# Kernel optimization log

Hardware: AMD Instinct MI355X
Metric: run time of the kernel (lower is better)

Reference implementation:

```python
import jax, jax.numpy as jnp
import numpy as np
from jax import lax

B, T_CAP, V, WD, H, L, IC = 256, 51, 10000, 512, 512, 2, 2048


def setup_inputs() -> dict:
    key = jax.random.key(0)
    ks = jax.random.split(key, 16)
    u01 = lambda k, s: jax.random.uniform(k, s, jnp.float32, -0.1, 0.1)
    sc = 1.0 / np.sqrt(H)
    uh = lambda k, s: jax.random.uniform(k, s, jnp.float32, -sc, sc)
    image_code = jax.random.normal(ks[0], (B, IC), jnp.float32)
    captions = jax.random.randint(ks[1], (B, T_CAP), 0, V)
    cap_lens = jax.random.randint(ks[2], (B,), 2, T_CAP + 1)
    cap_lens = cap_lens.at[0].set(T_CAP)  # guarantees max len == T_CAP (static scan length)
    return {
        "image_code": image_code,
        "captions": captions,
        "cap_lens": cap_lens,
        "embed_w": u01(ks[3], (V, WD)),
        "init_w": uh(ks[4], (L * H, IC)),
        "init_b": uh(ks[5], (L * H,)),
        "w_ih0": uh(ks[6], (3 * H, WD + IC)),
        "w_hh0": uh(ks[7], (3 * H, H)),
        "b_ih0": uh(ks[8], (3 * H,)),
        "b_hh0": uh(ks[9], (3 * H,)),
        "w_ih1": uh(ks[10], (3 * H, H)),
        "w_hh1": uh(ks[11], (3 * H, H)),
        "b_ih1": uh(ks[12], (3 * H,)),
        "b_hh1": uh(ks[13], (3 * H,)),
        "fc_w": u01(ks[14], (V, H)),
        "fc_b": jnp.zeros((V,), jnp.float32),
    }


def _gru_cell(x, h, w_ih, w_hh, b_ih, b_hh):
    # torch nn.GRU cell: gates ordered (r, z, n)
    gi = x @ w_ih.T + b_ih
    gh = h @ w_hh.T + b_hh
    i_r, i_z, i_n = jnp.split(gi, 3, axis=-1)
    h_r, h_z, h_n = jnp.split(gh, 3, axis=-1)
    r = jax.nn.sigmoid(i_r + h_r)
    z = jax.nn.sigmoid(i_z + h_z)
    n = jnp.tanh(i_n + r * h_n)
    return (1.0 - z) * n + z * h


def reference(image_code, captions, cap_lens, embed_w, init_w, init_b,
              w_ih0, w_hh0, b_ih0, b_hh0, w_ih1, w_hh1, b_ih1, b_hh1,
              fc_w, fc_b):
    b = image_code.shape[0]
    # sort by caption length, descending (ragged batch shrink in original)
    order = jnp.argsort(-cap_lens)
    sorted_lens = cap_lens[order]
    caps = captions[order]
    img = image_code[order]
    # init hidden: (L, B, H)
    h0 = (img @ init_w.T + init_b).reshape(b, L, H).transpose(1, 0, 2)
    lengths = sorted_lens - 1                      # decode steps per example
    T = captions.shape[1] - 1                      # static; equals lengths[0] by construction
    emb = embed_w[caps]                            # (B, T+1, WD)
    xs = jnp.swapaxes(emb[:, :T, :], 0, 1)         # (T, B, WD)
    mask_ts = jnp.arange(T)[:, None] < lengths[None, :]  # (T, B)
    params = [(w_ih0, w_hh0, b_ih0, b_hh0), (w_ih1, w_hh1, b_ih1, b_hh1)]

    def step(h, inp):
        x_emb, m = inp
        layer_in = jnp.concatenate([img, x_emb], axis=-1)  # (B, IC+WD)
        new_h = []
        for l, (wi, wh, bi, bh) in enumerate(params):
            hl = _gru_cell(layer_in, h[l], wi, wh, bi, bh)
            new_h.append(hl)
            layer_in = hl
        h_new = jnp.stack(new_h)
        # rows past their length keep their old hidden (equivalent to the
        # torch loop never touching rows beyond real_batch_size)
        h_new = jnp.where(m[None, :, None], h_new, h)
        preds = layer_in @ fc_w.T + fc_b           # dropout is identity in eval
        preds = jnp.where(m[:, None], preds, 0.0)  # predictions stay zero past length
        return h_new, preds

    _, preds = lax.scan(step, h0, (xs, mask_ts))   # preds: (T, B, V)
    predictions = jnp.swapaxes(preds, 0, 1)        # (B, T, V)
    return predictions, caps, lengths, order
```

## Files before the change

### kernel.cpp

```cpp
#include <hip/hip_runtime.h>
#include <hip/hip_bf16.h>

#define BB   256
#define TCAP 51
#define TT   50
#define VV   10000
#define WDIM 512
#define HH   512
#define ICC  2048
#define G3H  1536
#define FCP  8

typedef __attribute__((ext_vector_type(8))) short short8v;
typedef __attribute__((ext_vector_type(4))) float f32x4;

__device__ __forceinline__ unsigned short f2bf(float f) {
    unsigned u; __builtin_memcpy(&u, &f, 4);
    unsigned r = (u + 0x7FFFu + ((u >> 16) & 1u)) >> 16;
    return (unsigned short)r;
}
__device__ __forceinline__ float bf2f(unsigned short b) {
    unsigned u = ((unsigned)b) << 16; float f; __builtin_memcpy(&f, &u, 4); return f;
}
__device__ __forceinline__ short8v cvt8(float4 a, float4 b) {
    union { unsigned short u[8]; short8v v; } o;
    o.u[0] = f2bf(a.x); o.u[1] = f2bf(a.y); o.u[2] = f2bf(a.z); o.u[3] = f2bf(a.w);
    o.u[4] = f2bf(b.x); o.u[5] = f2bf(b.y); o.u[6] = f2bf(b.z); o.u[7] = f2bf(b.w);
    return o.v;
}
__device__ __forceinline__ float sigm(float x) { return 1.f / (1.f + expf(-x)); }

__global__ void sort_kernel(const int* __restrict__ cap_lens, const int* __restrict__ captions,
                            int* __restrict__ order_ws, int* __restrict__ len_ws,
                            int* __restrict__ caps_ws, float* __restrict__ out,
                            size_t predN) {
    __shared__ int s_order[BB];
    int i = threadIdx.x;
    int li = cap_lens[i];
    int rank = 0;
    for (int j = 0; j < BB; ++j) {
        int lj = cap_lens[j];
        rank += (lj > li) || (lj == li && j < i);
    }
    s_order[rank] = i;
    __syncthreads();
    int src = s_order[i];
    order_ws[i] = src;
    int len = cap_lens[src] - 1;
    len_ws[i] = len;
    for (int t = 0; t < TCAP; ++t) {
        int c = captions[src * TCAP + t];
        caps_ws[i * TCAP + t] = c;
        out[predN + (size_t)i * TCAP + t] = (float)c;
    }
    out[predN + (size_t)BB * TCAP + i]      = (float)len;
    out[predN + (size_t)BB * TCAP + BB + i] = (float)src;
}

__global__ void gather_imgb(const float* __restrict__ image_code, const int* __restrict__ order_ws,
                            unsigned short* __restrict__ imgb) {
    int i = blockIdx.x * 256 + threadIdx.x;
    int p = i >> 8, c8 = (i & 255) << 3;
    const float* s = image_code + (size_t)order_ws[p] * ICC + c8;
    float4 v0 = *(const float4*)s, v1 = *(const float4*)(s + 4);
    *(short8v*)&imgb[(size_t)p * ICC + c8] = cvt8(v0, v1);
}

__global__ void cvt_mat(const float* __restrict__ src, int src_ld, int src_off,
                        unsigned short* __restrict__ dst, int dst_ld, int dst_off,
                        int cols, int n8) {
    int i = blockIdx.x * 256 + threadIdx.x;
    if (i < n8) {
        int cpr = cols >> 3;
        int row = i / cpr, c8 = (i - row * cpr) << 3;
        const float* s = src + (size_t)row * src_ld + src_off + c8;
        float4 v0 = *(const float4*)s, v1 = *(const float4*)(s + 4);
        *(short8v*)&dst[(size_t)row * dst_ld + dst_off + c8] = cvt8(v0, v1);
    }
}

__global__ __launch_bounds__(256) void gemm_front(
    const unsigned short* __restrict__ imgb,
    const unsigned short* __restrict__ wcomb,
    const float* __restrict__ init_b,
    const float* __restrict__ b_ih0,
    unsigned short* __restrict__ h0s0,
    unsigned short* __restrict__ h1s0,
    float* __restrict__ gi_img) {
    const int p0 = blockIdx.y * 64;
    const int c0 = blockIdx.x * 64;
    const int tid = threadIdx.x;
    __shared__ unsigned short As[64][64 + FCP], Bs[64][64 + FCP];
    const int lane = tid & 63, w = tid >> 6;
    f32x4 acc[4] = {};
    for (int k0 = 0; k0 < ICC; k0 += 64) {
#pragma unroll
        for (int v = 0; v < 2; ++v) {
            int e = tid + v * 256;
            int rr = e >> 3, kk = (e & 7) * 8;
            *(short8v*)&As[rr][kk] = *(const short8v*)&imgb[(size_t)(p0 + rr) * ICC + k0 + kk];
            *(short8v*)&Bs[rr][kk] = *(const short8v*)&wcomb[(size_t)(c0 + rr) * ICC + k0 + kk];
        }
        __syncthreads();
#pragma unroll
        for (int ks = 0; ks < 64; ks += 32) {
            short8v a = *(const short8v*)&As[w * 16 + (lane & 15)][ks + (lane >> 4) * 8];
#pragma unroll
            for (int n = 0; n < 4; ++n) {
                short8v b = *(const short8v*)&Bs[n * 16 + (lane & 15)][ks + (lane >> 4) * 8];
                acc[n] = __builtin_amdgcn_mfma_f32_16x16x32_bf16(a, b, acc[n], 0, 0, 0);
            }
        }
        __syncthreads();
    }
#pragma unroll
    for (int n = 0; n < 4; ++n) {
        int cc = c0 + n * 16 + (lane & 15);
#pragma unroll
        for (int r = 0; r < 4; ++r) {
            int pr = p0 + w * 16 + (lane >> 4) * 4 + r;
            float v = acc[n][r];
            if (cc < 1024) {
                v += init_b[cc];
                unsigned short b = f2bf(v);
                if (cc < 512) h0s0[(size_t)pr * 512 + cc] = b;
                else          h1s0[(size_t)pr * 512 + (cc - 512)] = b;
            } else {
                gi_img[(size_t)pr * G3H + (cc - 1024)] = v + b_ih0[cc - 1024];
            }
        }
    }
}

__global__ __launch_bounds__(256) void gemm_giemb(
    const unsigned short* __restrict__ embb,
    const unsigned short* __restrict__ wihe,
    const float* __restrict__ gi_img,
    const int* __restrict__ caps_ws, const int* __restrict__ len_ws,
    float* __restrict__ gi_all) {
    const int r0 = blockIdx.y * 64;
    const int t = r0 >> 8, p0 = r0 & 255;
    if (len_ws[p0] <= t) return;
    const int c0 = blockIdx.x * 64;
    const int tid = threadIdx.x;
    __shared__ unsigned short As[64][64 + FCP], Bs[64][64 + FCP];
    __shared__ int s_arow[64];
    if (tid < 64) s_arow[tid] = caps_ws[(p0 + tid) * TCAP + t];
    __syncthreads();
    const int lane = tid & 63, w = tid >> 6;
    f32x4 acc[4] = {};
    for (int k0 = 0; k0 < WDIM; k0 += 64) {
#pragma unroll
        for (int v = 0; v < 2; ++v) {
            int e = tid + v * 256;
            int rr = e >> 3, kk = (e & 7) * 8;
            *(short8v*)&As[rr][kk] = *(const short8v*)&embb[(size_t)s_arow[rr] * WDIM + k0 + kk];
            *(short8v*)&Bs[rr][kk] = *(const short8v*)&wihe[(size_t)(c0 + rr) * WDIM + k0 + kk];
        }
        __syncthreads();
#pragma unroll
        for (int ks = 0; ks < 64; ks += 32) {
            short8v a = *(const short8v*)&As[w * 16 + (lane & 15)][ks + (lane >> 4) * 8];
#pragma unroll
            for (int n = 0; n < 4; ++n) {
                short8v b = *(const short8v*)&Bs[n * 16 + (lane & 15)][ks + (lane >> 4) * 8];
                acc[n] = __builtin_amdgcn_mfma_f32_16x16x32_bf16(a, b, acc[n], 0, 0, 0);
            }
        }
        __syncthreads();
    }
#pragma unroll
    for (int n = 0; n < 4; ++n) {
        int cc = c0 + n * 16 + (lane & 15);
#pragma unroll
        for (int r = 0; r < 4; ++r) {
            int pr = p0 + w * 16 + (lane >> 4) * 4 + r;
            if (t < len_ws[pr])
                gi_all[((size_t)t * BB + pr) * G3H + cc] = acc[n][r] + gi_img[(size_t)pr * G3H + cc];
        }
    }
}

__global__ __launch_bounds__(256) void gru_stage(int s,
    const unsigned short* __restrict__ h0_rd, unsigned short* __restrict__ h0_wr,
    float* __restrict__ gx_wr, const float* __restrict__ gx_rd,
    const unsigned short* __restrict__ h1_rd, unsigned short* __restrict__ h1_wr,
    unsigned short* __restrict__ h1x,
    const unsigned short* __restrict__ whh0b,
    const unsigned short* __restrict__ wih1b,
    const unsigned short* __restrict__ whh1b,
    const float* __restrict__ b_hh0, const float* __restrict__ gi_all,
    const float* __restrict__ b_ih1, const float* __restrict__ b_hh1,
    const int* __restrict__ len_ws) {
    const int role = blockIdx.x >> 5;
    const int sub = blockIdx.x & 31;
    const int cc0 = (sub & 7) * 64;
    const int p0 = (sub >> 3) * 64;
    const int t = s - role;
    if (t < 0 || t >= TT) return;
    if (len_ws[p0] <= t) return;
    const int tid = threadIdx.x, lane = tid & 63, w = tid >> 6;
    __shared__ unsigned short As[64][72];
    __shared__ unsigned short Bs[3][64][72];
    const unsigned short* Arows = (role == 2) ? h1_rd : h0_rd;
    const unsigned short* Bw = (role == 0) ? whh0b : (role == 1) ? wih1b : whh1b;
    const int rr0 = tid >> 3, kk0 = (tid & 7) * 8;
    f32x4 aG0[4] = {}, aG1[4] = {}, aG2[4] = {};
    short8v pa0, pa1, pb00, pb01, pb02, pb10, pb11, pb12;

#define LOADK(KC) {                                                                  \
    size_t ko = (size_t)(KC) * 64 + kk0;                                             \
    pa0  = *(const short8v*)&Arows[(size_t)(p0 + rr0) * 512 + ko];                   \
    pa1  = *(const short8v*)&Arows[(size_t)(p0 + rr0 + 32) * 512 + ko];              \
    pb00 = *(const short8v*)&Bw[(size_t)(cc0 + rr0) * 512 + ko];                     \
    pb01 = *(const short8v*)&Bw[(size_t)(512 + cc0 + rr0) * 512 + ko];               \
    pb02 = *(const short8v*)&Bw[(size_t)(1024 + cc0 + rr0) * 512 + ko];              \
    pb10 = *(const short8v*)&Bw[(size_t)(cc0 + rr0 + 32) * 512 + ko];                \
    pb11 = *(const short8v*)&Bw[(size_t)(512 + cc0 + rr0 + 32) * 512 + ko];          \
    pb12 = *(const short8v*)&Bw[(size_t)(1024 + cc0 + rr0 + 32) * 512 + ko]; }

    LOADK(0);
    for (int kc = 0; kc < 8; ++kc) {
        if (kc) __syncthreads();
        *(short8v*)&As[rr0][kk0] = pa0;
        *(short8v*)&As[rr0 + 32][kk0] = pa1;
        *(short8v*)&Bs[0][rr0][kk0] = pb00;
        *(short8v*)&Bs[1][rr0][kk0] = pb01;
        *(short8v*)&Bs[2][rr0][kk0] = pb02;
        *(short8v*)&Bs[0][rr0 + 32][kk0] = pb10;
        *(short8v*)&Bs[1][rr0 + 32][kk0] = pb11;
        *(short8v*)&Bs[2][rr0 + 32][kk0] = pb12;
        __syncthreads();
        if (kc < 7) LOADK(kc + 1);
#pragma unroll
        for (int ks = 0; ks < 64; ks += 32) {
            short8v a = *(const short8v*)&As[w * 16 + (lane & 15)][ks + (lane >> 4) * 8];
#pragma unroll
            for (int n = 0; n < 4; ++n) {
                int br = n * 16 + (lane & 15), bk = ks + (lane >> 4) * 8;
                short8v b0 = *(const short8v*)&Bs[0][br][bk];
                aG0[n] = __builtin_amdgcn_mfma_f32_16x16x32_bf16(a, b0, aG0[n], 0, 0, 0);
                short8v b1 = *(const short8v*)&Bs[1][br][bk];
                aG1[n] = __builtin_amdgcn_mfma_f32_16x16x32_bf16(a, b1, aG1[n], 0, 0, 0);
                short8v b2 = *(const short8v*)&Bs[2][br][bk];
                aG2[n] = __builtin_amdgcn_mfma_f32_16x16x32_bf16(a, b2, aG2[n], 0, 0, 0);
            }
        }
    }
#undef LOADK

    if (role == 0) {
#pragma unroll
        for (int n = 0; n < 4; ++n) {
            int cc = cc0 + n * 16 + (lane & 15);
            float bR = b_hh0[cc], bZ = b_hh0[512 + cc], bN = b_hh0[1024 + cc];
#pragma unroll
            for (int r = 0; r < 4; ++r) {
                int p = p0 + w * 16 + (lane >> 4) * 4 + r;
                const float* gi = gi_all + ((size_t)t * BB + p) * G3H;
                float rr_ = sigm(gi[cc] + aG0[n][r] + bR);
                float zz  = sigm(gi[512 + cc] + aG1[n][r] + bZ);
                float nn  = tanhf(gi[1024 + cc] + rr_ * (aG2[n][r] + bN));
                float hold = bf2f(h0_rd[(size_t)p * 512 + cc]);
                float hnew = (t < len_ws[p]) ? (1.f - zz) * nn + zz * hold : hold;
                h0_wr[(size_t)p * 512 + cc] = f2bf(hnew);
            }
        }
    } else if (role == 1) {
#pragma unroll
        for (int n = 0; n < 4; ++n) {
            int cc = cc0 + n * 16 + (lane & 15);
            float bR = b_ih1[cc], bZ = b_ih1[512 + cc], bN = b_ih1[1024 + cc];
#pragma unroll
            for (int r = 0; r < 4; ++r) {
                int p = p0 + w * 16 + (lane >> 4) * 4 + r;
                float* gx = gx_wr + (size_t)p * G3H;
                gx[cc]        = aG0[n][r] + bR;
                gx[512 + cc]  = aG1[n][r] + bZ;
                gx[1024 + cc] = aG2[n][r] + bN;
            }
        }
    } else {
#pragma unroll
        for (int n = 0; n < 4; ++n) {
            int cc = cc0 + n * 16 + (lane & 15);
            float bR = b_hh1[cc], bZ = b_hh1[512 + cc], bN = b_hh1[1024 + cc];
#pragma unroll
            for (int r = 0; r < 4; ++r) {
                int p = p0 + w * 16 + (lane >> 4) * 4 + r;
                const float* gx = gx_rd + (size_t)p * G3H;
                float rr_ = sigm(gx[cc] + aG0[n][r] + bR);
                float zz  = sigm(gx[512 + cc] + aG1[n][r] + bZ);
                float nn  = tanhf(gx[1024 + cc] + rr_ * (aG2[n][r] + bN));
                float hold = bf2f(h1_rd[(size_t)p * 512 + cc]);
                float hnew = (t < len_ws[p]) ? (1.f - zz) * nn + zz * hold : hold;
                unsigned short hb = f2bf(hnew);
                h1_wr[(size_t)p * 512 + cc] = hb;
                h1x[((size_t)t * BB + p) * 512 + cc] = hb;
            }
        }
    }
}

__global__ __launch_bounds__(256) void gemm_fc_mfma(
    const unsigned short* __restrict__ h1x,
    const unsigned short* __restrict__ fcwb,
    const float* __restrict__ fc_b,
    const int* __restrict__ len_ws,
    float* __restrict__ out) {
    const int r0 = blockIdx.y * 64;
    const int t = r0 >> 8, p0 = r0 & 255;
    const int c0 = blockIdx.x * 64;
    const int tid = threadIdx.x;
    if (len_ws[p0] <= t) {
        for (int e = tid; e < 64 * 16; e += 256) {
            int rl = e >> 4, c = c0 + (e & 15) * 4;
            if (c < VV) {
                float4 z = {0.f, 0.f, 0.f, 0.f};
                *(float4*)&out[((size_t)(p0 + rl) * TT + t) * VV + c] = z;
            }
        }
        return;
    }
    __shared__ unsigned short As[64][64 + FCP];
    __shared__ unsigned short Bs[64][64 + FCP];
    const int lane = tid & 63, w = tid >> 6;
    f32x4 acc[4] = {};
    for (int k0 = 0; k0 < HH; k0 += 64) {
#pragma unroll
        for (int v = 0; v < 2; ++v) {
            int e = tid + v * 256;
            int rr = e >> 3, kk = (e & 7) * 8;
            *(short8v*)&As[rr][kk] =
                *(const short8v*)&h1x[((size_t)(t * BB + p0 + rr)) * HH + k0 + kk];
            int bc = c0 + rr;
            short8v bv = {};
            if (bc < VV) bv = *(const short8v*)&fcwb[(size_t)bc * HH + k0 + kk];
            *(short8v*)&Bs[rr][kk] = bv;
        }
        __syncthreads();
#pragma unroll
        for (int ks = 0; ks < 64; ks += 32) {
            short8v a = *(const short8v*)&As[w * 16 + (lane & 15)][ks + (lane >> 4) * 8];
#pragma unroll
            for (int n = 0; n < 4; ++n) {
                short8v b = *(const short8v*)&Bs[n * 16 + (lane & 15)][ks + (lane >> 4) * 8];
                acc[n] = __builtin_amdgcn_mfma_f32_16x16x32_bf16(a, b, acc[n], 0, 0, 0);
            }
        }
        __syncthreads();
    }
#pragma unroll
    for (int n = 0; n < 4; ++n) {
        int c = c0 + n * 16 + (lane & 15);
        if (c < VV) {
            float bias = fc_b[c];
#pragma unroll
            for (int r = 0; r < 4; ++r) {
                int pr = p0 + w * 16 + (lane >> 4) * 4 + r;
                bool act = (t < len_ws[pr]);
                out[((size_t)pr * TT + t) * VV + c] = act ? (acc[n][r] + bias) : 0.f;
            }
        }
    }
}

extern "C" void kernel_launch(void* const* d_in, const int* in_sizes, int n_in,
                              void* d_out, int out_size, void* d_ws, size_t ws_size,
                              hipStream_t stream) {
    const float* image_code = (const float*)d_in[0];
    const int*   captions   = (const int*)d_in[1];
    const int*   cap_lens   = (const int*)d_in[2];
    const float* embed_w    = (const float*)d_in[3];
    const float* init_w     = (const float*)d_in[4];
    const float* init_b     = (const float*)d_in[5];
    const float* w_ih0      = (const float*)d_in[6];
    const float* w_hh0      = (const float*)d_in[7];
    const float* b_ih0      = (const float*)d_in[8];
    const float* b_hh0      = (const float*)d_in[9];
    const float* w_ih1      = (const float*)d_in[10];
    const float* w_hh1      = (const float*)d_in[11];
    const float* b_ih1      = (const float*)d_in[12];
    const float* b_hh1      = (const float*)d_in[13];
    const float* fc_w       = (const float*)d_in[14];
    const float* fc_b       = (const float*)d_in[15];
    float* out = (float*)d_out;

    const size_t tail = (size_t)BB * TCAP + 2 * BB;
    const size_t predN = (size_t)out_size - tail;

    char* ws = (char*)d_ws;
    int*   order_ws = (int*)(ws + 0);
    int*   len_ws   = (int*)(ws + 1024);
    int*   caps_ws  = (int*)(ws + 2048);
    unsigned short* h0s[2] = {(unsigned short*)(ws + 54272),  (unsigned short*)(ws + 316416)};
    unsigned short* h1s[2] = {(unsigned short*)(ws + 578560), (unsigned short*)(ws + 840704)};
    float* gxb[2] = {(float*)(ws + 1102848), (float*)(ws + 2675712)};
    float* gi_img   = (float*)(ws + 4248576);
    float* gi_all   = (float*)(ws + 5821440);
    unsigned short* h1x  = (unsigned short*)(ws + 84464640);
    unsigned short* fcwb = (unsigned short*)(ws + 97571840);

    char* ob = (char*)d_out;
    unsigned short* imgb   = (unsigned short*)(ob + 0);
    unsigned short* wihe   = (unsigned short*)(ob + 1048576);
    unsigned short* wcomb  = (unsigned short*)(ob + 4194304);
    unsigned short* embb   = (unsigned short*)(ob + 16777216);
    unsigned short* whh0b  = (unsigned short*)(ob + 27262976);
    unsigned short* wih1b  = (unsigned short*)(ob + 29360128);
    unsigned short* whh1b  = (unsigned short*)(ob + 31457280);

    dim3 blk(256);
    hipLaunchKernelGGL(sort_kernel, dim3(1), blk, 0, stream,
                       cap_lens, captions, order_ws, len_ws, caps_ws, out, predN);
    hipLaunchKernelGGL(gather_imgb, dim3(256), blk, 0, stream, image_code, order_ws, imgb);
    hipLaunchKernelGGL(cvt_mat, dim3(1024), blk, 0, stream,
                       init_w, ICC, 0, wcomb, ICC, 0, ICC, 1024 * ICC / 8);
    hipLaunchKernelGGL(cvt_mat, dim3(1536), blk, 0, stream,
                       w_ih0, ICC + WDIM, 0, wcomb + (size_t)1024 * ICC, ICC, 0, ICC, G3H * ICC / 8);
    hipLaunchKernelGGL(cvt_mat, dim3(384), blk, 0, stream,
                       w_ih0, ICC + WDIM, ICC, wihe, WDIM, 0, WDIM, G3H * WDIM / 8);
    hipLaunchKernelGGL(cvt_mat, dim3(2500), blk, 0, stream,
                       embed_w, WDIM, 0, embb, WDIM, 0, WDIM, VV * WDIM / 8);
    hipLaunchKernelGGL(cvt_mat, dim3(2500), blk, 0, stream,
                       fc_w, WDIM, 0, fcwb, WDIM, 0, WDIM, VV * WDIM / 8);
    hipLaunchKernelGGL(cvt_mat, dim3(384), blk, 0, stream,
                       w_hh0, WDIM, 0, whh0b, WDIM, 0, WDIM, G3H * WDIM / 8);
    hipLaunchKernelGGL(cvt_mat, dim3(384), blk, 0, stream,
                       w_ih1, WDIM, 0, wih1b, WDIM, 0, WDIM, G3H * WDIM / 8);
    hipLaunchKernelGGL(cvt_mat, dim3(384), blk, 0, stream,
                       w_hh1, WDIM, 0, whh1b, WDIM, 0, WDIM, G3H * WDIM / 8);

    hipLaunchKernelGGL(gemm_front, dim3(40, 4), blk, 0, stream,
                       imgb, wcomb, init_b, b_ih0, h0s[0], h1s[0], gi_img);
    hipLaunchKernelGGL(gemm_giemb, dim3(24, 200), blk, 0, stream,
                       embb, wihe, gi_img, caps_ws, len_ws, gi_all);

    for (int s = 0; s <= TT + 1; ++s) {
        int q = s & 1;
        hipLaunchKernelGGL(gru_stage, dim3(96), blk, 0, stream, s,
                           h0s[q], h0s[q ^ 1],
                           gxb[q ^ 1], gxb[q],
                           h1s[q], h1s[q ^ 1],
                           h1x, whh0b, wih1b, whh1b,
                           b_hh0, gi_all, b_ih1, b_hh1, len_ws);
    }

    hipLaunchKernelGGL(gemm_fc_mfma, dim3(157, 200), blk, 0, stream,
                       h1x, fcwb, fc_b, len_ws, out);
}
```

Measured before the change: 1.353 ms.

## Keep FC weight slice resident in LDS and stream rows through it

The final vocabulary projection GEMM is restructured. Each block now loads a full 32-column by 512-K slice of the bf16 FC weights into XOR-swizzled shared memory once, then loops over 8 groups of 64 output rows, reading A fragments straight from global memory into registers. This replaces the 64x64 tile with per-K-step global-to-LDS staging and barriers, removing repeated weight reloads and syncs. The cost is a narrower output tile, so column stores are less coalesced, plus higher register use for the 16 A fragments.

```diff
diff --git a/kernel.cpp b/kernel.cpp
--- a/kernel.cpp
+++ b/kernel.cpp
@@ -302,65 +302,71 @@
     }
 }
 
-__global__ __launch_bounds__(256) void gemm_fc_mfma(
+__global__ __launch_bounds__(256) void gemm_fc_bres(
     const unsigned short* __restrict__ h1x,
     const unsigned short* __restrict__ fcwb,
     const float* __restrict__ fc_b,
     const int* __restrict__ len_ws,
     float* __restrict__ out) {
-    const int r0 = blockIdx.y * 64;
-    const int t = r0 >> 8, p0 = r0 & 255;
-    const int c0 = blockIdx.x * 64;
-    const int tid = threadIdx.x;
-    if (len_ws[p0] <= t) {
-        for (int e = tid; e < 64 * 16; e += 256) {
-            int rl = e >> 4, c = c0 + (e & 15) * 4;
-            if (c < VV) {
-                float4 z = {0.f, 0.f, 0.f, 0.f};
-                *(float4*)&out[((size_t)(p0 + rl) * TT + t) * VV + c] = z;
-            }
-        }
-        return;
-    }
-    __shared__ unsigned short As[64][64 + FCP];
-    __shared__ unsigned short Bs[64][64 + FCP];
-    const int lane = tid & 63, w = tid >> 6;
-    f32x4 acc[4] = {};
-    for (int k0 = 0; k0 < HH; k0 += 64) {
-#pragma unroll
-        for (int v = 0; v < 2; ++v) {
-            int e = tid + v * 256;
-            int rr = e >> 3, kk = (e & 7) * 8;
-            *(short8v*)&As[rr][kk] =
-                *(const short8v*)&h1x[((size_t)(t * BB + p0 + rr)) * HH + k0 + kk];
-            int bc = c0 + rr;
-            short8v bv = {};
-            if (bc < VV) bv = *(const short8v*)&fcwb[(size_t)bc * HH + k0 + kk];
-            *(short8v*)&Bs[rr][kk] = bv;
-        }
-        __syncthreads();
-#pragma unroll
-        for (int ks = 0; ks < 64; ks += 32) {
-            short8v a = *(const short8v*)&As[w * 16 + (lane & 15)][ks + (lane >> 4) * 8];
-#pragma unroll
-            for (int n = 0; n < 4; ++n) {
-                short8v b = *(const short8v*)&Bs[n * 16 + (lane & 15)][ks + (lane >> 4) * 8];
-                acc[n] = __builtin_amdgcn_mfma_f32_16x16x32_bf16(a, b, acc[n], 0, 0, 0);
-            }
-        }
-        __syncthreads();
-    }
-#pragma unroll
-    for (int n = 0; n < 4; ++n) {
-        int c = c0 + n * 16 + (lane & 15);
-        if (c < VV) {
-            float bias = fc_b[c];
-#pragma unroll
-            for (int r = 0; r < 4; ++r) {
-                int pr = p0 + w * 16 + (lane >> 4) * 4 + r;
-                bool act = (t < len_ws[pr]);
-                out[((size_t)pr * TT + t) * VV + c] = act ? (acc[n][r] + bias) : 0.f;
-            }
+    const int c0 = blockIdx.x * 32;
+    const int R0 = blockIdx.y * 512;
+    const int tid = threadIdx.x, lane = tid & 63, w = tid >> 6;
+    __shared__ unsigned short Bsm[32 * 512];
+
+#pragma unroll
+    for (int v = 0; v < 8; ++v) {
+        int e = tid + v * 256;
+        int r = e >> 6, c = e & 63;
+        short8v bv = {};
+        if (c0 + r < VV) bv = *(const short8v*)&fcwb[(size_t)(c0 + r) * 512 + c * 8];
+        *(short8v*)&Bsm[r * 512 + (c ^ (r & 7)) * 8] = bv;
+    }
+    __syncthreads();
+
+    const float bias0 = (c0 + (lane & 15) < VV) ? fc_b[c0 + (lane & 15)] : 0.f;
+    const float bias1 = (c0 + 16 + (lane & 15) < VV) ? fc_b[c0 + 16 + (lane & 15)] : 0.f;
+
+#pragma unroll
+    for (int rg = 0; rg < 8; ++rg) {
+        const int rowbase = R0 + rg * 64;
+        const int t = rowbase >> 8;
+        const int prg = rowbase & 255;
+        const int arow = rowbase + w * 16 + (lane & 15);
+        if (len_ws[prg] <= t) {
+#pragma unroll
+            for (int v = 0; v < 8; ++v) {
+                int e = tid + v * 256;
+                int rl = e >> 5, cl = e & 31;
+                int c = c0 + cl;
+                if (c < VV) {
+                    int grow = rowbase + rl;
+                    out[((size_t)(grow & 255) * TT + (grow >> 8)) * VV + c] = 0.f;
+                }
+            }
+            continue;
+        }
+        short8v af[16];
+#pragma unroll
+        for (int ks = 0; ks < 16; ++ks)
+            af[ks] = *(const short8v*)&h1x[(size_t)arow * 512 + ks * 32 + (lane >> 4) * 8];
+        f32x4 acc0 = {}, acc1 = {};
+#pragma unroll
+        for (int ks = 0; ks < 16; ++ks) {
+            int cb = ks * 4 + (lane >> 4);
+            int br0 = lane & 15, br1 = 16 + (lane & 15);
+            short8v b0 = *(const short8v*)&Bsm[br0 * 512 + (cb ^ (br0 & 7)) * 8];
+            acc0 = __builtin_amdgcn_mfma_f32_16x16x32_bf16(af[ks], b0, acc0, 0, 0, 0);
+            short8v b1 = *(const short8v*)&Bsm[br1 * 512 + (cb ^ (br1 & 7)) * 8];
+            acc1 = __builtin_amdgcn_mfma_f32_16x16x32_bf16(af[ks], b1, acc1, 0, 0, 0);
+        }
+        int cA = c0 + (lane & 15), cB = c0 + 16 + (lane & 15);
+#pragma unroll
+        for (int r = 0; r < 4; ++r) {
+            int grow = rowbase + w * 16 + (lane >> 4) * 4 + r;
+            int p = grow & 255, tt = grow >> 8;
+            bool act = (tt < len_ws[p]);
+            if (cA < VV) out[((size_t)p * TT + tt) * VV + cA] = act ? (acc0[r] + bias0) : 0.f;
+            if (cB < VV) out[((size_t)p * TT + tt) * VV + cB] = act ? (acc1[r] + bias1) : 0.f;
         }
     }
 }
@@ -446,6 +452,6 @@
                            b_hh0, gi_all, b_ih1, b_hh1, len_ws);
     }
 
-    hipLaunchKernelGGL(gemm_fc_mfma, dim3(157, 200), blk, 0, stream,
+    hipLaunchKernelGGL(gemm_fc_bres, dim3(313, 25), blk, 0, stream,
                        h1x, fcwb, fc_b, len_ws, out);
 }
```

Result: slower. 1.447 ms (+7.0%).
